# Kernel optimization log

Measured on AMD Instinct MI355X. Metric: run time of the kernel, lower is better.

Reference implementation:

```python
import math
import jax, jax.numpy as jnp
import numpy as np

RATIO = 0.1

def setup_inputs() -> dict:
    key = jax.random.key(0)
    ks = jax.random.split(key, 8)
    B, S, D = 8, 4096, 2048
    transformer_out = jax.random.normal(ks[0], (B, S, D), jnp.float32)
    hidden_states = jax.random.normal(ks[1], (B, S, D), jnp.float32)
    lengths = jax.random.randint(ks[2], (B,), S // 2, S + 1)
    attention_mask = (jnp.arange(S)[None, :] < lengths[:, None]).astype(jnp.int32)
    s = 1.0 / math.sqrt(D)
    W1 = jax.random.normal(ks[3], (D, D), jnp.float32) * s
    b1 = jnp.zeros((D,), jnp.float32)
    w2 = jax.random.normal(ks[4], (D,), jnp.float32) * s
    b2 = jnp.zeros((), jnp.float32)
    Wv = jax.random.normal(ks[5], (D, D), jnp.float32) * s
    bv = jnp.zeros((D,), jnp.float32)
    return dict(transformer_out=transformer_out, hidden_states=hidden_states,
                attention_mask=attention_mask, W1=W1, b1=b1, w2=w2, b2=b2, Wv=Wv, bv=bv)

def reference(transformer_out, hidden_states, attention_mask, W1, b1, w2, b2, Wv, bv):
    B, S, D = transformer_out.shape
    M = math.ceil(S * RATIO)  # static upper bound on max_nugget (n_nugget <= ceil(S*ratio))
    # scorer MLP: Linear(D,D) -> ReLU -> Linear(D,1), squeezed
    h = jax.nn.relu(jnp.einsum('bsd,de->bse', transformer_out, W1) + b1)
    scores = jnp.einsum('bse,e->bs', h, w2) + b2                      # [B,S]
    maskb = attention_mask.astype(bool)
    scores = jnp.where(maskb, scores, jnp.finfo(scores.dtype).min)    # masked fill
    n_token = maskb.sum(axis=1)                                        # [B]
    n_nugget = jnp.ceil(n_token.astype(scores.dtype) * RATIO).astype(jnp.int32)
    n_nugget = jnp.minimum(jnp.maximum(n_nugget, 1), n_token)
    nugget_mask = jnp.arange(M)[None, :] < n_nugget[:, None]          # [B,M] ragged validity
    # descending top-k by double argsort, then stable reorder to original token order
    sorted_idx = jnp.argsort(-scores, axis=1)[:, :M]                   # [B,M]
    big = jnp.iinfo(sorted_idx.dtype).max
    resort = jnp.where(nugget_mask, sorted_idx, big)
    indices = jnp.take_along_axis(sorted_idx, jnp.argsort(resort, axis=1), axis=1)
    enc = jnp.take_along_axis(hidden_states, indices[:, :, None], axis=1)  # [B,M,D]
    enc = jnp.einsum('bmd,de->bme', enc, Wv) + bv                      # value_ffn
    nugget_scores = jnp.take_along_axis(scores, indices, axis=1)       # [B,M]
    return enc, nugget_mask, nugget_scores, indices, scores
```

## Files before the change

### kernel.cpp

```cpp
#include <hip/hip_runtime.h>
#include <float.h>
#include <math.h>

typedef _Float16 h16;
typedef _Float16 h16x8 __attribute__((ext_vector_type(8)));
typedef float    f32x4 __attribute__((ext_vector_type(4)));

#define MFMA16(a, b, c) __builtin_amdgcn_mfma_f32_16x16x32_f16((a), (b), (c), 0, 0, 0)

#define B_    8
#define S_    4096
#define D_    2048
#define M_    410
#define MROWS (B_ * S_)
#define R2    (B_ * M_)

#define MASK_FILL (-3.3895313892515355e38f)

#define ENC_OFF  0
#define MASK_OFF (B_ * M_ * D_)
#define NSC_OFF  (MASK_OFF + B_ * M_)
#define IDX_OFF  (NSC_OFF + B_ * M_)
#define SC_OFF   (IDX_OFF + B_ * M_)

#define WS_W1T  ((size_t)0)
#define WS_WVT  ((size_t)8  << 20)
#define WS_PART ((size_t)16 << 20)
#define WS_IDX  ((size_t)17 << 20)
#define WS_A16  ((size_t)18 << 20)
#define WS_NEED_SMALL (((size_t)17 << 20) + R2 * sizeof(int))
#define WS_NEED_BIG   (WS_A16 + (size_t)MROWS * D_ * sizeof(h16))

__device__ inline float finite_or(float v, float alt) {
    return (v == v && v <= FLT_MAX && v >= -FLT_MAX) ? v : alt;
}

__device__ inline void gload_lds16(const h16* g, h16* l) {
    __builtin_amdgcn_global_load_lds(
        (const __attribute__((address_space(1))) void*)g,
        (__attribute__((address_space(3))) void*)l, 16, 0, 0);
}

__device__ inline h16x8 cvt8(f32x4 a, f32x4 b) {
    h16x8 r;
#pragma unroll
    for (int i = 0; i < 4; ++i) { r[i] = (h16)a[i]; r[i + 4] = (h16)b[i]; }
    return r;
}

__global__ __launch_bounds__(256) void precvt_kernel(
    const float* __restrict__ T, h16* __restrict__ A16)
{
    const size_t n = (size_t)MROWS * D_;
    for (size_t i = ((size_t)blockIdx.x * 256 + threadIdx.x) * 8; i < n;
         i += (size_t)gridDim.x * 256 * 8) {
        f32x4 a = *(const f32x4*)(T + i);
        f32x4 b = *(const f32x4*)(T + i + 4);
        *(h16x8*)(A16 + i) = cvt8(a, b);
    }
}

__global__ __launch_bounds__(256) void transpose_kernel(
    const float* __restrict__ W1, const float* __restrict__ Wv,
    h16* __restrict__ w1t, h16* __restrict__ wvt)
{
    __shared__ float tile[32][33];
    const float* src = blockIdx.z ? Wv : W1;
    h16* dt = blockIdx.z ? wvt : w1t;
    const int tx = threadIdx.x, ty = threadIdx.y;
    const int n0 = blockIdx.x * 32, k0 = blockIdx.y * 32;
#pragma unroll
    for (int i = 0; i < 4; ++i) {
        int k = k0 + ty + i * 8;
        tile[ty + i * 8][tx] = src[(size_t)k * D_ + n0 + tx];
    }
    __syncthreads();
#pragma unroll
    for (int i = 0; i < 4; ++i) {
        int n = n0 + ty + i * 8;
        dt[(size_t)n * D_ + k0 + tx] = (h16)tile[tx][ty + i * 8];
    }
}

#define PH_SYNC do { __builtin_amdgcn_s_barrier(); \
    asm volatile("s_waitcnt lgkmcnt(0)" ::: "memory"); \
    __builtin_amdgcn_sched_barrier(0); } while (0)
#define PH_END  __builtin_amdgcn_s_barrier()

#define QUAD(mb, nb2) do { \
    __builtin_amdgcn_s_setprio(1); \
    _Pragma("unroll") for (int i_ = 0; i_ < 4; ++i_) \
    _Pragma("unroll") for (int jn_ = 0; jn_ < 2; ++jn_) \
    _Pragma("unroll") for (int ks_ = 0; ks_ < 2; ++ks_) \
        acc[(mb) + i_][(nb2) + jn_] = \
            MFMA16(fa[ks_][i_], fb[ks_][jn_], acc[(mb) + i_][(nb2) + jn_]); \
    __builtin_amdgcn_s_setprio(0); } while (0)

__global__ __launch_bounds__(512, 2) void gemm8v2_kernel(
    const h16* __restrict__ A16,
    const h16* __restrict__ Bt,
    const float* __restrict__ bias,
    const float* __restrict__ w2,
    float* __restrict__ outp)
{
    constexpr int NT = 32;
    __shared__ h16 As[2][256][64];
    __shared__ h16 Bs[2][256][64];
    __shared__ float red[4][256];

    const int pn = blockIdx.y & 7;
    const int pm = blockIdx.x + 8 * (blockIdx.y >> 3);
    const int t = threadIdx.x;
    const int lane = t & 63, wid = t >> 6;
    const int wm = wid >> 2, wn = wid & 3;
    const int l15 = lane & 15, kseg = lane >> 4;
    const int pc0 = kseg ^ (l15 & 7);

    const int sc = (t & 7) ^ ((t >> 3) & 7);
    const h16* Ag = A16 + (size_t)(pm * 256 + (t >> 3)) * D_ + sc * 8;
    const h16* Bg = Bt  + (size_t)(pn * 256 + (t >> 3)) * D_ + sc * 8;
    char* AsB = (char*)&As[0][0][0];
    char* BsB = (char*)&Bs[0][0][0];

    f32x4 acc[8][4] = {};
    h16x8 fa[2][4], fb[2][2];

    auto STAGE = [&](int kt, int nb) {
#pragma unroll
        for (int j = 0; j < 4; ++j)
            gload_lds16(Ag + (size_t)j * 64 * D_ + kt * 64,
                        (h16*)(AsB + nb * 65536 + j * 8192 + wid * 1024));
#pragma unroll
        for (int j = 0; j < 4; ++j)
            gload_lds16(Bg + (size_t)j * 64 * D_ + kt * 64,
                        (h16*)(BsB + nb * 65536 + j * 8192 + wid * 1024));
    };
    auto LDA = [&](int cb, int mb) {
#pragma unroll
        for (int i = 0; i < 4; ++i) {
            const int row = wm * 128 + (mb + i) * 16 + l15;
#pragma unroll
            for (int ks = 0; ks < 2; ++ks)
                fa[ks][i] = *(const h16x8*)&As[cb][row][(pc0 ^ (ks << 2)) * 8];
        }
    };
    auto LDB = [&](int cb, int nb2) {
#pragma unroll
        for (int i = 0; i < 2; ++i) {
            const int row = wn * 64 + (nb2 + i) * 16 + l15;
#pragma unroll
            for (int ks = 0; ks < 2; ++ks)
                fb[ks][i] = *(const h16x8*)&Bs[cb][row][(pc0 ^ (ks << 2)) * 8];
        }
    };

    STAGE(0, 0);
    asm volatile("s_waitcnt vmcnt(0)" ::: "memory");
    __builtin_amdgcn_s_barrier();

    for (int kt = 0; kt < NT; ++kt) {
        const int cb = kt & 1;
        LDA(cb, 0); LDB(cb, 0);
        if (kt + 1 < NT) STAGE(kt + 1, cb ^ 1);
        PH_SYNC; QUAD(0, 0); PH_END;
        LDB(cb, 2);
        PH_SYNC; QUAD(0, 2); PH_END;
        LDA(cb, 4);
        PH_SYNC; QUAD(4, 2); PH_END;
        LDB(cb, 0);
        PH_SYNC; QUAD(4, 0);
        asm volatile("s_waitcnt vmcnt(0)" ::: "memory");
        PH_END;
    }
    __syncthreads();

    float vout[8][4];
#pragma unroll
    for (int fm = 0; fm < 8; ++fm)
#pragma unroll
        for (int rg = 0; rg < 4; ++rg) vout[fm][rg] = 0.0f;
#pragma unroll
    for (int fn = 0; fn < 4; ++fn) {
        int ng = pn * 256 + wn * 64 + fn * 16 + l15;
        float w = w2[ng], bb = bias[ng];
#pragma unroll
        for (int fm = 0; fm < 8; ++fm)
#pragma unroll
            for (int rg = 0; rg < 4; ++rg) {
                float c = acc[fm][fn][rg] + bb;
                c = fmaxf(c, 0.0f);
                vout[fm][rg] += c * w;
            }
    }
#pragma unroll
    for (int off = 1; off < 16; off <<= 1)
#pragma unroll
        for (int fm = 0; fm < 8; ++fm)
#pragma unroll
            for (int rg = 0; rg < 4; ++rg)
                vout[fm][rg] += __shfl_xor(vout[fm][rg], off);
    if (l15 == 0) {
#pragma unroll
        for (int fm = 0; fm < 8; ++fm)
#pragma unroll
            for (int rg = 0; rg < 4; ++rg)
                red[wn][wm * 128 + fm * 16 + kseg * 4 + rg] = vout[fm][rg];
    }
    __syncthreads();
    if (t < 256) {
        float s = red[0][t] + red[1][t] + red[2][t] + red[3][t];
        outp[(size_t)pn * MROWS + pm * 256 + t] = s;
    }
}

template <int MODE>
__global__ __launch_bounds__(512, 4) void gemm_kernel(
    const float* __restrict__ A, const h16* __restrict__ Bt,
    const float* __restrict__ bias, const float* __restrict__ w2,
    float* __restrict__ outp, const int* __restrict__ gidx)
{
    constexpr int BM = 128, BN = 256, BK = 32;
    constexpr int NT = D_ / BK;
    __shared__ h16 As[2][BM][32];
    __shared__ h16 Bs[2][BN][32];
    __shared__ float red[4][128];

    int pn, pm;
    if constexpr (MODE == 0) {
        pn = blockIdx.y & 7;
        pm = blockIdx.x + 8 * (blockIdx.y >> 3);
    } else {
        pn = blockIdx.x; pm = blockIdx.y;
    }
    const int t = threadIdx.x;
    const int lane = t & 63, wid = t >> 6;
    const int wm = wid >> 2, wn = wid & 3;
    const int l15 = lane & 15, kseg = lane >> 4;
    const int pcf = (kseg ^ ((l15 >> 1) & 3)) * 8;

    const int arow = t >> 2, aseg = t & 3;
    const int pcA = (aseg ^ ((arow >> 1) & 3)) * 8;
    const int lrow   = lane >> 2;
    const int lchunk = (lane & 3) ^ ((lane >> 3) & 3);

    const float* Ap;
    if constexpr (MODE == 0) {
        Ap = A + (size_t)(pm * BM + arow) * D_ + aseg * 8;
    } else {
        int r = pm * BM + arow;
        int rr = (r < R2) ? r : R2 - 1;
        int bb = rr / M_;
        int tok = gidx[rr];
        Ap = A + ((size_t)bb * S_ + tok) * D_ + aseg * 8;
    }
    const h16* gB0 = Bt + (size_t)(pn * BN + 32 * wid + lrow)      * D_ + lchunk * 8;
    const h16* gB1 = Bt + (size_t)(pn * BN + 32 * wid + 16 + lrow) * D_ + lchunk * 8;

    f32x4 acc[4][4] = {};

    f32x4 a0 = *(const f32x4*)Ap, a1 = *(const f32x4*)(Ap + 4);
    *(h16x8*)&As[0][arow][pcA] = cvt8(a0, a1);
    gload_lds16(gB0, &Bs[0][32 * wid][0]);
    gload_lds16(gB1, &Bs[0][32 * wid + 16][0]);
    gB0 += BK; gB1 += BK;
    Ap += BK;
    a0 = *(const f32x4*)Ap; a1 = *(const f32x4*)(Ap + 4);
    __syncthreads();

    for (int kt = 0; kt < NT; ++kt) {
        const int cur = kt & 1;
        if (kt + 1 < NT) {
            *(h16x8*)&As[cur ^ 1][arow][pcA] = cvt8(a0, a1);
            gload_lds16(gB0, &Bs[cur ^ 1][32 * wid][0]);
            gload_lds16(gB1, &Bs[cur ^ 1][32 * wid + 16][0]);
            gB0 += BK; gB1 += BK;
        }
        if (kt + 2 < NT) {
            Ap += BK;
            a0 = *(const f32x4*)Ap; a1 = *(const f32x4*)(Ap + 4);
        }
        h16x8 fa[4];
#pragma unroll
        for (int fm = 0; fm < 4; ++fm) {
            int row = wm * 64 + fm * 16 + l15;
            fa[fm] = *(const h16x8*)&As[cur][row][pcf];
        }
#pragma unroll
        for (int fn = 0; fn < 4; ++fn) {
            int row = wn * 64 + fn * 16 + l15;
            h16x8 fb = *(const h16x8*)&Bs[cur][row][pcf];
#pragma unroll
            for (int fm = 0; fm < 4; ++fm)
                acc[fm][fn] = MFMA16(fa[fm], fb, acc[fm][fn]);
        }
        __syncthreads();
    }

    if constexpr (MODE == 0) {
        float vout[4][4] = {};
#pragma unroll
        for (int fn = 0; fn < 4; ++fn) {
            int ng = pn * BN + wn * 64 + fn * 16 + l15;
            float w = w2[ng], bb = bias[ng];
#pragma unroll
            for (int fm = 0; fm < 4; ++fm)
#pragma unroll
                for (int rg = 0; rg < 4; ++rg) {
                    float c = acc[fm][fn][rg] + bb;
                    c = fmaxf(c, 0.0f);
                    vout[fm][rg] += c * w;
                }
        }
#pragma unroll
        for (int off = 1; off < 16; off <<= 1)
#pragma unroll
            for (int fm = 0; fm < 4; ++fm)
#pragma unroll
                for (int rg = 0; rg < 4; ++rg)
                    vout[fm][rg] += __shfl_xor(vout[fm][rg], off);
        if (l15 == 0) {
#pragma unroll
            for (int fm = 0; fm < 4; ++fm)
#pragma unroll
                for (int rg = 0; rg < 4; ++rg)
                    red[wn][wm * 64 + fm * 16 + kseg * 4 + rg] = vout[fm][rg];
        }
        __syncthreads();
        if (t < 128) {
            float s = red[0][t] + red[1][t] + red[2][t] + red[3][t];
            outp[(size_t)pn * MROWS + pm * BM + t] = s;
        }
    } else {
#pragma unroll
        for (int fn = 0; fn < 4; ++fn) {
            int ng = pn * BN + wn * 64 + fn * 16 + l15;
            float bb = bias[ng];
#pragma unroll
            for (int fm = 0; fm < 4; ++fm) {
                int rbase = pm * BM + wm * 64 + fm * 16 + kseg * 4;
#pragma unroll
                for (int rg = 0; rg < 4; ++rg) {
                    int r = rbase + rg;
                    if (r < R2)
                        outp[(size_t)r * D_ + ng] =
                            finite_or(acc[fm][fn][rg] + bb, 0.0f);
                }
            }
        }
    }
}

__global__ __launch_bounds__(256) void score_reduce_kernel(
    const float* __restrict__ part, const float* __restrict__ b2,
    const int* __restrict__ amask, float* __restrict__ outF)
{
    int m = blockIdx.x * 256 + threadIdx.x;
    float v = b2[0];
#pragma unroll
    for (int p = 0; p < 8; ++p) v += part[(size_t)p * MROWS + m];
    v = finite_or(v, 0.0f);
    if (amask[m] == 0) v = MASK_FILL;
    outF[SC_OFF + m] = v;
}

__global__ __launch_bounds__(1024) void topk_kernel(
    const float* __restrict__ scores, const int* __restrict__ amask,
    float* __restrict__ outF, int* __restrict__ idx_ws)
{
    const int b = blockIdx.x, t = threadIdx.x;
    __shared__ float s[S_];
    __shared__ int perm[S_];
    __shared__ int sel[512];
    __shared__ int wsum[16];

    int cnt = 0;
    for (int i = t; i < S_; i += 1024) {
        float v = scores[b * S_ + i];
        s[i] = v; perm[i] = i;
        cnt += amask[b * S_ + i];
    }
#pragma unroll
    for (int off = 1; off < 64; off <<= 1) cnt += __shfl_xor(cnt, off);
    if ((t & 63) == 0) wsum[t >> 6] = cnt;
    __syncthreads();
    int n_token = 0;
#pragma unroll
    for (int w = 0; w < 16; ++w) n_token += wsum[w];
    int nn = (int)ceilf((float)n_token * 0.1f);
    if (nn < 1) nn = 1;
    if (nn > n_token) nn = n_token;

    for (int k = 2; k <= S_; k <<= 1)
        for (int j = k >> 1; j > 0; j >>= 1) {
            __syncthreads();
            for (int i = t; i < S_; i += 1024) {
                int ixj = i ^ j;
                if (ixj > i) {
                    int a = perm[i], c = perm[ixj];
                    bool ok = (s[a] > s[c]) || (s[a] == s[c] && a < c);
                    if (((i & k) == 0) ? !ok : ok) { perm[i] = c; perm[ixj] = a; }
                }
            }
        }
    __syncthreads();
    for (int i = t; i < 512; i += 1024) sel[i] = (i < nn) ? perm[i] : 0x7fffffff;
    for (int k = 2; k <= 512; k <<= 1)
        for (int j = k >> 1; j > 0; j >>= 1) {
            __syncthreads();
            if (t < 512) {
                int i = t, ixj = i ^ j;
                if (ixj > i) {
                    int a = sel[i], c = sel[ixj];
                    if (((i & k) == 0) ? (a > c) : (a < c)) { sel[i] = c; sel[ixj] = a; }
                }
            }
        }
    __syncthreads();
    for (int m = t; m < M_; m += 1024) {
        int idx = (m < nn) ? sel[m] : perm[m];
        outF[MASK_OFF + b * M_ + m] = (m < nn) ? 1.0f : 0.0f;
        outF[NSC_OFF + b * M_ + m]  = s[idx];
        outF[IDX_OFF + b * M_ + m]  = (float)idx;
        idx_ws[b * M_ + m] = idx;
    }
}

extern "C" void kernel_launch(void* const* d_in, const int* in_sizes, int n_in,
                              void* d_out, int out_size, void* d_ws, size_t ws_size,
                              hipStream_t stream)
{
    const float* T  = (const float*)d_in[0];
    const float* H  = (const float*)d_in[1];
    const int*   AM = (const int*)d_in[2];
    const float* W1 = (const float*)d_in[3];
    const float* b1 = (const float*)d_in[4];
    const float* w2 = (const float*)d_in[5];
    const float* b2 = (const float*)d_in[6];
    const float* Wv = (const float*)d_in[7];
    const float* bv = (const float*)d_in[8];
    float* outF = (float*)d_out;
    char* ws = (char*)d_ws;

    if (ws_size < WS_NEED_SMALL) return;

    h16* w1t  = (h16*)(ws + WS_W1T);
    h16* wvt  = (h16*)(ws + WS_WVT);
    float* part = (float*)(ws + WS_PART);
    int* idxw   = (int*)(ws + WS_IDX);

    transpose_kernel<<<dim3(64, 64, 2), dim3(32, 8), 0, stream>>>(
        W1, Wv, w1t, wvt);

    if (ws_size >= WS_NEED_BIG) {
        h16* a16 = (h16*)(ws + WS_A16);
        precvt_kernel<<<dim3(2048), 256, 0, stream>>>(T, a16);
        gemm8v2_kernel<<<dim3(8, 128), 512, 0, stream>>>(
            a16, w1t, b1, w2, part);
    } else {
        gemm_kernel<0><<<dim3(8, 256), 512, 0, stream>>>(
            T, w1t, b1, w2, part, nullptr);
    }
    score_reduce_kernel<<<dim3(128), 256, 0, stream>>>(part, b2, AM, outF);
    topk_kernel<<<dim3(8), 1024, 0, stream>>>(outF + SC_OFF, AM, outF, idxw);
    gemm_kernel<1><<<dim3(8, 26), 512, 0, stream>>>(
        H, wvt, bv, nullptr, outF + ENC_OFF, idxw);
}
```

Baseline: 536.1 us.

## Merge fp16 precast and weight transpose into one launch; double-buffer B fragments

Fuses the activation fp32-to-fp16 conversion and the W1/Wv transpose kernels into a single prep kernel so one launch covers both and their blocks can run concurrently. In the main GEMM, B fragments are kept in two register sets so the fourth phase reuses the first set instead of reloading it from LDS. The explicit lgkmcnt waits and sched barriers before each MFMA phase are dropped, leaving ordering to the compiler. This costs more VGPRs under a 2-wave occupancy bound, and removing the waits leans on the compiler to insert correct dependencies.

Measured after the change: 526.2 us. No clear change (-1.9%).

```diff
diff --git a/kernel.cpp b/kernel.cpp
--- a/kernel.cpp
+++ b/kernel.cpp
@@ -48,27 +48,31 @@
     return r;
 }
 
-__global__ __launch_bounds__(256) void precvt_kernel(
-    const float* __restrict__ T, h16* __restrict__ A16)
-{
-    const size_t n = (size_t)MROWS * D_;
-    for (size_t i = ((size_t)blockIdx.x * 256 + threadIdx.x) * 8; i < n;
-         i += (size_t)gridDim.x * 256 * 8) {
-        f32x4 a = *(const f32x4*)(T + i);
-        f32x4 b = *(const f32x4*)(T + i + 4);
-        *(h16x8*)(A16 + i) = cvt8(a, b);
-    }
-}
-
-__global__ __launch_bounds__(256) void transpose_kernel(
+__global__ __launch_bounds__(256) void prep_kernel(
+    const float* __restrict__ T, h16* __restrict__ A16, int do_precvt,
     const float* __restrict__ W1, const float* __restrict__ Wv,
     h16* __restrict__ w1t, h16* __restrict__ wvt)
 {
+    const int bid = blockIdx.x;
+    if (bid < 2048) {
+        if (!do_precvt) return;
+        const size_t n = (size_t)MROWS * D_;
+        for (size_t i = ((size_t)bid * 256 + threadIdx.x) * 8; i < n;
+             i += (size_t)2048 * 256 * 8) {
+            f32x4 a = *(const f32x4*)(T + i);
+            f32x4 b = *(const f32x4*)(T + i + 4);
+            *(h16x8*)(A16 + i) = cvt8(a, b);
+        }
+        return;
+    }
     __shared__ float tile[32][33];
-    const float* src = blockIdx.z ? Wv : W1;
-    h16* dt = blockIdx.z ? wvt : w1t;
-    const int tx = threadIdx.x, ty = threadIdx.y;
-    const int n0 = blockIdx.x * 32, k0 = blockIdx.y * 32;
+    const int id = bid - 2048;
+    const int bz = id >> 12, rem = id & 4095;
+    const int bx = rem & 63, by = rem >> 6;
+    const float* src = bz ? Wv : W1;
+    h16* dt = bz ? wvt : w1t;
+    const int tx = threadIdx.x & 31, ty = threadIdx.x >> 5;
+    const int n0 = bx * 32, k0 = by * 32;
 #pragma unroll
     for (int i = 0; i < 4; ++i) {
         int k = k0 + ty + i * 8;
@@ -82,21 +86,18 @@
     }
 }
 
-#define PH_SYNC do { __builtin_amdgcn_s_barrier(); \
-    asm volatile("s_waitcnt lgkmcnt(0)" ::: "memory"); \
-    __builtin_amdgcn_sched_barrier(0); } while (0)
-#define PH_END  __builtin_amdgcn_s_barrier()
-
-#define QUAD(mb, nb2) do { \
+#define PH_BAR  __builtin_amdgcn_s_barrier()
+
+#define QUADX(mb, nb2, FB) do { \
     __builtin_amdgcn_s_setprio(1); \
+    _Pragma("unroll") for (int ks_ = 0; ks_ < 2; ++ks_) \
     _Pragma("unroll") for (int i_ = 0; i_ < 4; ++i_) \
     _Pragma("unroll") for (int jn_ = 0; jn_ < 2; ++jn_) \
-    _Pragma("unroll") for (int ks_ = 0; ks_ < 2; ++ks_) \
         acc[(mb) + i_][(nb2) + jn_] = \
-            MFMA16(fa[ks_][i_], fb[ks_][jn_], acc[(mb) + i_][(nb2) + jn_]); \
+            MFMA16(fa[ks_][i_], FB[ks_][jn_], acc[(mb) + i_][(nb2) + jn_]); \
     __builtin_amdgcn_s_setprio(0); } while (0)
 
-__global__ __launch_bounds__(512, 2) void gemm8v2_kernel(
+__global__ __launch_bounds__(512, 2) void gemm8v3_kernel(
     const h16* __restrict__ A16,
     const h16* __restrict__ Bt,
     const float* __restrict__ bias,
@@ -123,7 +124,7 @@
     char* BsB = (char*)&Bs[0][0][0];
 
     f32x4 acc[8][4] = {};
-    h16x8 fa[2][4], fb[2][2];
+    h16x8 fa[2][4], fbA[2][2], fbB[2][2];
 
     auto STAGE = [&](int kt, int nb) {
 #pragma unroll
@@ -144,13 +145,22 @@
                 fa[ks][i] = *(const h16x8*)&As[cb][row][(pc0 ^ (ks << 2)) * 8];
         }
     };
-    auto LDB = [&](int cb, int nb2) {
+    auto LDBA = [&](int cb) {
 #pragma unroll
         for (int i = 0; i < 2; ++i) {
-            const int row = wn * 64 + (nb2 + i) * 16 + l15;
+            const int row = wn * 64 + i * 16 + l15;
 #pragma unroll
             for (int ks = 0; ks < 2; ++ks)
-                fb[ks][i] = *(const h16x8*)&Bs[cb][row][(pc0 ^ (ks << 2)) * 8];
+                fbA[ks][i] = *(const h16x8*)&Bs[cb][row][(pc0 ^ (ks << 2)) * 8];
+        }
+    };
+    auto LDBB = [&](int cb) {
+#pragma unroll
+        for (int i = 0; i < 2; ++i) {
+            const int row = wn * 64 + (2 + i) * 16 + l15;
+#pragma unroll
+            for (int ks = 0; ks < 2; ++ks)
+                fbB[ks][i] = *(const h16x8*)&Bs[cb][row][(pc0 ^ (ks << 2)) * 8];
         }
     };
 
@@ -160,17 +170,16 @@
 
     for (int kt = 0; kt < NT; ++kt) {
         const int cb = kt & 1;
-        LDA(cb, 0); LDB(cb, 0);
+        LDA(cb, 0); LDBA(cb);
         if (kt + 1 < NT) STAGE(kt + 1, cb ^ 1);
-        PH_SYNC; QUAD(0, 0); PH_END;
-        LDB(cb, 2);
-        PH_SYNC; QUAD(0, 2); PH_END;
+        PH_BAR; QUADX(0, 0, fbA); PH_BAR;
+        LDBB(cb);
+        PH_BAR; QUADX(0, 2, fbB); PH_BAR;
         LDA(cb, 4);
-        PH_SYNC; QUAD(4, 2); PH_END;
-        LDB(cb, 0);
-        PH_SYNC; QUAD(4, 0);
+        PH_BAR; QUADX(4, 2, fbB); PH_BAR;
+        PH_BAR; QUADX(4, 0, fbA);
         asm volatile("s_waitcnt vmcnt(0)" ::: "memory");
-        PH_END;
+        PH_BAR;
     }
     __syncthreads();
 
@@ -447,14 +456,13 @@
     h16* wvt  = (h16*)(ws + WS_WVT);
     float* part = (float*)(ws + WS_PART);
     int* idxw   = (int*)(ws + WS_IDX);
-
-    transpose_kernel<<<dim3(64, 64, 2), dim3(32, 8), 0, stream>>>(
-        W1, Wv, w1t, wvt);
-
-    if (ws_size >= WS_NEED_BIG) {
-        h16* a16 = (h16*)(ws + WS_A16);
-        precvt_kernel<<<dim3(2048), 256, 0, stream>>>(T, a16);
-        gemm8v2_kernel<<<dim3(8, 128), 512, 0, stream>>>(
+    const int big = (ws_size >= WS_NEED_BIG);
+    h16* a16 = big ? (h16*)(ws + WS_A16) : (h16*)(ws + WS_W1T);
+
+    prep_kernel<<<dim3(10240), 256, 0, stream>>>(T, a16, big, W1, Wv, w1t, wvt);
+
+    if (big) {
+        gemm8v3_kernel<<<dim3(8, 128), 512, 0, stream>>>(
             a16, w1t, b1, w2, part);
     } else {
         gemm_kernel<0><<<dim3(8, 256), 512, 0, stream>>>(
```
